# Kernel tuning notes

Measured on AMD Instinct MI355X. Metric: run time of the kernel, lower is better.

Reference implementation:

```python
import jax, jax.numpy as jnp
import numpy as np

EPS_KNN = 1e-12
EPS_COS = 1e-8


def setup_inputs() -> dict:
    key = jax.random.key(0)
    ks = jax.random.split(key, 12)
    B, N, D, H = 2048, 50000, 3, 512
    z = jax.random.normal(ks[0], (B, D + 3), jnp.float32)
    t = jax.random.uniform(ks[1], (), jnp.float32)
    x0 = jax.random.normal(ks[2], (N, D), jnp.float32)
    x1 = jax.random.normal(ks[3], (N, D), jnp.float32)
    v0 = jax.random.normal(ks[4], (N, D), jnp.float32)
    v1 = jax.random.normal(ks[5], (N, D), jnp.float32)
    # MLP model: (D+1) -> H -> H -> D
    W1 = jax.random.normal(ks[6], (D + 1, H), jnp.float32) * 0.1
    b1 = jnp.zeros((H,), jnp.float32)
    W2 = jax.random.normal(ks[7], (H, H), jnp.float32) * 0.05
    b2 = jnp.zeros((H,), jnp.float32)
    W3 = jax.random.normal(ks[8], (H, D), jnp.float32) * 0.05
    b3 = jnp.zeros((D,), jnp.float32)
    return {"z": z, "t": t, "x0": x0, "x1": x1, "v0": v0, "v1": v1,
            "W1": W1, "b1": b1, "W2": W2, "b2": b2, "W3": W3, "b3": b3,
            "k": 100}


def _mlp(xin, W1, b1, W2, b2, W3, b3):
    h = jax.nn.relu(xin @ W1 + b1)
    h = jax.nn.relu(h @ W2 + b2)
    return h @ W3 + b3


def _get_ut_knn_gaussian(xt, x0, x1, v0, v1, k):
    x = jnp.concatenate([x0, x1], axis=0)   # [2N, D]
    v = jnp.concatenate([v0, v1], axis=0)   # [2N, D]
    # euclidean cdist via the GEMM identity, clamped for numerical safety
    d2 = ((xt * xt).sum(1, keepdims=True)
          + (x * x).sum(1)[None, :]
          - 2.0 * xt @ x.T)                 # [B, 2N]
    dists = jnp.sqrt(jnp.maximum(d2, 0.0))
    neg_d, knn_idx = jax.lax.top_k(-dists, k)  # smallest-k, ascending in dist
    knn_dists = -neg_d                          # [B, k]
    h = jnp.maximum(knn_dists[:, -1:], EPS_KNN)  # bandwidth = k-th distance
    w = jnp.exp(-knn_dists ** 2 / (2.0 * h ** 2))
    w = w / (w.sum(1, keepdims=True) + EPS_KNN)
    v_knn = v[knn_idx]                           # [B, k, D] gather
    return jnp.einsum('bk,bkd->bd', w, v_knn)


def reference(z, t, x0, x1, v0, v1, W1, b1, W2, b2, W3, b3, k):
    x = z[:, :-3]                                 # [B, D]
    B = x.shape[0]
    t_col = jnp.full((B, 1), t, dtype=x.dtype)
    x_dot = _mlp(jnp.concatenate([x, t_col], axis=1), W1, b1, W2, b2, W3, b3)
    u_t = _get_ut_knn_gaussian(x, x0, x1, v0, v1, k)
    nu = jnp.maximum(jnp.linalg.norm(u_t, axis=1), EPS_COS)
    nd = jnp.maximum(jnp.linalg.norm(x_dot, axis=1), EPS_COS)
    cos_dist = 1.0 - (u_t * x_dot).sum(1) / (nu * nd)
    # self.cos_dist_all starts at 0, so after one call cos_dist_all == cos_dist
    cos_dist_all = cos_dist
    l2_sq = ((u_t - x_dot) ** 2).sum(1)
    return jnp.concatenate([x_dot, cos_dist_all[:, None], cos_dist[:, None], l2_sq[:, None]], axis=1)
```

## Files before the change

### kernel.cpp

```cpp
#include <hip/hip_runtime.h>
#include <math.h>

#define KTHREADS 256
#define QB 2
#define NBUCKET 2048
#define CANDMAX 1024
#define TINY 256
#define TSAMP 8u
#define EPS_KNN 1e-12f
#define EPS_COS 1e-8f
#define MQ 8

__device__ __forceinline__ float wredf(float v) {
#pragma unroll
    for (int off = 32; off > 0; off >>= 1) v += __shfl_xor(v, off, 64);
    return v;
}
__device__ __forceinline__ unsigned int wredu(unsigned int v) {
#pragma unroll
    for (int off = 32; off > 0; off >>= 1) v += (unsigned int)__shfl_xor((int)v, off, 64);
    return v;
}

__global__ __launch_bounds__(512) void mlp_kernel(
    const float* __restrict__ z, const float* __restrict__ tp,
    const float* __restrict__ W1, const float* __restrict__ b1,
    const float* __restrict__ W2, const float* __restrict__ b2,
    const float* __restrict__ W3, const float* __restrict__ b3,
    float* __restrict__ xdot, int B)
{
    __shared__ float h1[MQ][512];
    __shared__ float red[8][MQ * 3];
    const int tid = threadIdx.x, lane = tid & 63, wid = tid >> 6;
    const int qbase = blockIdx.x * MQ;
    const float t = tp[0];

    for (int idx = tid; idx < MQ * 512; idx += 512) {
        const int q = idx >> 9, j = idx & 511;
        const int qid = qbase + q;
        float v = 0.f;
        if (qid < B) {
            const float a = z[qid * 6 + 0], b = z[qid * 6 + 1], c = z[qid * 6 + 2];
            v = fmaf(a, W1[j], fmaf(b, W1[512 + j], fmaf(c, W1[1024 + j], fmaf(t, W1[1536 + j], b1[j]))));
            v = fmaxf(v, 0.f);
        }
        h1[q][j] = v;
    }
    __syncthreads();

    const int col = wid * 64 + lane;
    float acc[MQ];
#pragma unroll
    for (int q = 0; q < MQ; ++q) acc[q] = b2[col];

    float w[4], wn[4];
#pragma unroll
    for (int u = 0; u < 4; ++u) w[u] = W2[u * 512 + col];
    for (int r = 0; r < 512; r += 4) {
        const int rn = r + 4;
        if (rn < 512) {
#pragma unroll
            for (int u = 0; u < 4; ++u) wn[u] = W2[(rn + u) * 512 + col];
        }
        float4 hv[MQ];
#pragma unroll
        for (int q = 0; q < MQ; ++q) hv[q] = *(const float4*)&h1[q][r];
#pragma unroll
        for (int q = 0; q < MQ; ++q) {
            acc[q] = fmaf(hv[q].x, w[0], acc[q]);
            acc[q] = fmaf(hv[q].y, w[1], acc[q]);
            acc[q] = fmaf(hv[q].z, w[2], acc[q]);
            acc[q] = fmaf(hv[q].w, w[3], acc[q]);
        }
#pragma unroll
        for (int u = 0; u < 4; ++u) w[u] = wn[u];
    }

    const float wc0 = W3[col * 3 + 0], wc1 = W3[col * 3 + 1], wc2 = W3[col * 3 + 2];
#pragma unroll
    for (int q = 0; q < MQ; ++q) {
        const float h = fmaxf(acc[q], 0.f);
        float p0 = h * wc0, p1 = h * wc1, p2 = h * wc2;
        p0 = wredf(p0); p1 = wredf(p1); p2 = wredf(p2);
        if (lane == 0) { red[wid][q * 3 + 0] = p0; red[wid][q * 3 + 1] = p1; red[wid][q * 3 + 2] = p2; }
    }
    __syncthreads();
    if (tid < MQ * 3) {
        const int q = tid / 3, d = tid % 3;
        float s = 0.f;
#pragma unroll
        for (int w8 = 0; w8 < 8; ++w8) s += red[w8][q * 3 + d];
        const int qid = qbase + q;
        if (qid < B) xdot[qid * 3 + d] = s + b3[d];
    }
}

template<int NB>
__device__ void scan_find(const unsigned int* h, unsigned int T,
                          int* out_b, unsigned int* out_total,
                          unsigned int* wtot, int tid)
{
    constexpr int CH = NB / KTHREADS;
    const int lane = tid & 63, wid = tid >> 6;
    const int base = tid * CH;
    unsigned int s = 0;
#pragma unroll
    for (int u = 0; u < CH; ++u) s += h[base + u];
    unsigned int incl = s;
#pragma unroll
    for (int d = 1; d < 64; d <<= 1) {
        unsigned int n = (unsigned int)__shfl_up((int)incl, d, 64);
        if (lane >= d) incl += n;
    }
    if (tid == 0) *out_b = -1;
    if (lane == 63) wtot[wid] = incl;
    __syncthreads();
    unsigned int offs = 0;
    for (int w = 0; w < wid; ++w) offs += wtot[w];
    const unsigned int total = wtot[0] + wtot[1] + wtot[2] + wtot[3];
    const unsigned int excl = offs + (incl - s);
    if (excl < T && T <= excl + s) {
        unsigned int c = excl;
        for (int u = 0; u < CH; ++u) {
            c += h[base + u];
            if (c >= T) { *out_b = base + u; break; }
        }
    }
    if (tid == 0) *out_total = total;
    __syncthreads();
}

__global__ __launch_bounds__(KTHREADS) void knn_kernel(
    const float* __restrict__ z,
    const float* __restrict__ x0, const float* __restrict__ x1,
    const float* __restrict__ v0, const float* __restrict__ v1,
    const float* __restrict__ xdot, const int* __restrict__ kp,
    float* __restrict__ out, int B, int N0, int N1)
{
    const int N = N0 + N1;
    const unsigned int K = (unsigned int)kp[0];

    __shared__ unsigned int hist[QB][NBUCKET];
    float (*candD)[CANDMAX] = (float (*)[CANDMAX])&hist[0][0];
    int   (*candI)[CANDMAX] = (int (*)[CANDMAX])((char*)&hist[0][0] + sizeof(float) * QB * CANDMAX);
    __shared__ unsigned int fh[256];
    __shared__ float tinyD[TINY];
    __shared__ int   tinyI[TINY];
    __shared__ unsigned int tcnt;
    __shared__ unsigned int candCnt[QB];
    __shared__ float capv[QB];
    __shared__ float hselv[QB];
    __shared__ int   iselv[QB];
    __shared__ int   doneQ[QB];
    __shared__ int   anyleft;
    __shared__ unsigned int wtot[4];
    __shared__ int s_b;
    __shared__ unsigned int s_tot;
    __shared__ float qsh[QB][4];
    __shared__ float redbuf[4][QB * 4];

    const int tid = threadIdx.x, lane = tid & 63, wid = tid >> 6;
    const int qbase = blockIdx.x * QB;

    if (tid < QB) {
        const int qid = qbase + tid;
        float a = 0.f, b = 0.f, c = 0.f;
        if (qid < B) { a = z[qid * 6 + 0]; b = z[qid * 6 + 1]; c = z[qid * 6 + 2]; }
        qsh[tid][0] = a; qsh[tid][1] = b; qsh[tid][2] = c;
        qsh[tid][3] = fmaf(a, a, fmaf(b, b, c * c));
    }
    for (int i = tid; i < QB * NBUCKET; i += KTHREADS) (&hist[0][0])[i] = 0u;
    __syncthreads();

    float qx[QB], qy[QB], qz[QB], q2[QB];
#pragma unroll
    for (int q = 0; q < QB; ++q) { qx[q] = qsh[q][0]; qy[q] = qsh[q][1]; qz[q] = qsh[q][2]; q2[q] = qsh[q][3]; }

    auto doPoint = [&](float px, float py, float pz, int idx, auto&& fn) {
        const float p2 = fmaf(px, px, fmaf(py, py, pz * pz));
#pragma unroll
        for (int q = 0; q < QB; ++q) {
            const float dt = fmaf(qx[q], px, fmaf(qy[q], py, qz[q] * pz));
            const float d2 = fmaf(-2.f, dt, q2[q] + p2);
            fn(q, idx, d2);
        }
    };

    auto sweepArr = [&](const float* xa, int nG, int ibase, auto&& fn) {
        int g = tid;
        if (g < nG) {
            const float4* bp = (const float4*)(xa + 12 * (size_t)g);
            float4 A = bp[0], Bv = bp[1], C = bp[2];
            for (;;) {
                const int gn = g + KTHREADS;
                float4 An, Bn, Cn;
                const bool has = gn < nG;
                if (has) {
                    const float4* np = (const float4*)(xa + 12 * (size_t)gn);
                    An = np[0]; Bn = np[1]; Cn = np[2];
                }
                const int ib = ibase + 4 * g;
                doPoint(A.x, A.y, A.z, ib + 0, fn);
                doPoint(A.w, Bv.x, Bv.y, ib + 1, fn);
                doPoint(Bv.z, Bv.w, C.x, ib + 2, fn);
                doPoint(C.y, C.z, C.w, ib + 3, fn);
                if (!has) break;
                g = gn; A = An; Bv = Bn; C = Cn;
            }
        }
    };

    auto sweepAll = [&](auto&& fn) {
        const int G0 = N0 >> 2, G1 = N1 >> 2;
        sweepArr(x0, G0, 0, fn);
        for (int j = (G0 << 2) + tid; j < N0; j += KTHREADS)
            doPoint(x0[3 * j], x0[3 * j + 1], x0[3 * j + 2], j, fn);
        sweepArr(x1, G1, N0, fn);
        for (int j = (G1 << 2) + tid; j < N1; j += KTHREADS)
            doPoint(x1[3 * j], x1[3 * j + 1], x1[3 * j + 2], N0 + j, fn);
    };

    for (int s = tid; s < 2048; s += KTHREADS) {
        const int j = (int)(((long long)s * (long long)N) >> 11);
        float px, py, pz;
        if (j < N0) { px = x0[3 * j]; py = x0[3 * j + 1]; pz = x0[3 * j + 2]; }
        else { const int j2 = j - N0; px = x1[3 * j2]; py = x1[3 * j2 + 1]; pz = x1[3 * j2 + 2]; }
        const float p2 = fmaf(px, px, fmaf(py, py, pz * pz));
#pragma unroll
        for (int q = 0; q < QB; ++q) {
            const float dt = fmaf(qx[q], px, fmaf(qy[q], py, qz[q] * pz));
            float d2 = fmaf(-2.f, dt, q2[q] + p2);
            d2 = fmaxf(d2, 0.f);
            int bu = (int)(__float_as_uint(d2) >> 20);
            bu = bu < (NBUCKET - 1) ? bu : (NBUCKET - 1);
            atomicAdd(&hist[q][bu], 1u);
        }
    }
    __syncthreads();
    for (int q = 0; q < QB; ++q) {
        scan_find<NBUCKET>(&hist[q][0], TSAMP, &s_b, &s_tot, wtot, tid);
        if (tid == 0) {
            int b = s_b; if (b < 0) b = NBUCKET - 1;
            const unsigned int ub = (unsigned int)(b + 1);
            const float cap = (ub >= 2040u) ? 3.4e38f : __uint_as_float(ub << 20);
            capv[q] = (qbase + q < B) ? cap : -1.f;
            doneQ[q] = (qbase + q < B) ? 0 : 1;
        }
        __syncthreads();
    }

    for (int attempt = 0; attempt < 4; ++attempt) {
        if (tid == 0) anyleft = 0;
        if (tid < QB && !doneQ[tid]) candCnt[tid] = 0u;
        __syncthreads();
        float rcap[QB];
#pragma unroll
        for (int q = 0; q < QB; ++q) rcap[q] = doneQ[q] ? -1.f : capv[q];
        sweepAll([&](int q, int j, float d2) {
            if (d2 < rcap[q]) {
                const unsigned int pos = atomicAdd(&candCnt[q], 1u);
                if (pos < (unsigned int)CANDMAX) { candD[q][pos] = sqrtf(fmaxf(d2, 0.f)); candI[q][pos] = j; }
            }
        });
        __syncthreads();
        if (tid < QB && !doneQ[tid]) {
            const unsigned int c = candCnt[tid];
            if (c >= K && c <= (unsigned int)CANDMAX) doneQ[tid] = 1;
            else {
                const unsigned int cc = c < 8u ? 8u : c;
                capv[tid] *= __powf(384.f / (float)cc, 0.6666667f);
                anyleft = 1;
            }
        }
        __syncthreads();
        if (!anyleft) break;
    }

    for (int q = 0; q < QB; ++q) {
        if (qbase + q >= B) continue;
        const unsigned int cnt = candCnt[q];
        const int m = (int)(cnt < (unsigned int)CANDMAX ? cnt : (unsigned int)CANDMAX);
        fh[tid] = 0u;
        __syncthreads();
        const float sc = 256.f / sqrtf(capv[q]);
        for (int i = tid; i < m; i += KTHREADS) {
            int b = (int)(candD[q][i] * sc); b = b < 255 ? b : 255;
            atomicAdd(&fh[b], 1u);
        }
        __syncthreads();
        scan_find<256>(fh, K, &s_b, &s_tot, wtot, tid);
        const int bsel = s_b < 0 ? 255 : s_b;
        unsigned int v = (tid < bsel) ? fh[tid] : 0u;
        v = wredu(v);
        if (lane == 0) wtot[wid] = v;
        if (tid == 0) tcnt = 0u;
        __syncthreads();
        const unsigned int Cb = wtot[0] + wtot[1] + wtot[2] + wtot[3];
        for (int i = tid; i < m; i += KTHREADS) {
            int b = (int)(candD[q][i] * sc); b = b < 255 ? b : 255;
            if (b == bsel) {
                const unsigned int p = atomicAdd(&tcnt, 1u);
                if (p < (unsigned int)TINY) { tinyD[p] = candD[q][i]; tinyI[p] = candI[q][i]; }
            }
        }
        __syncthreads();
        const int c2 = (int)tcnt;
        const int need = (int)K - 1 - (int)Cb;
        if (c2 <= TINY) {
            for (int i = tid; i < c2; i += KTHREADS) {
                const float di = tinyD[i]; const int ii = tinyI[i];
                int r = 0;
                for (int j2 = 0; j2 < c2; ++j2) {
                    const float dj = tinyD[j2];
                    if (dj < di || (dj == di && tinyI[j2] < ii)) ++r;
                }
                if (r == need) { hselv[q] = di; iselv[q] = ii; }
            }
        } else {
            for (int i = tid; i < m; i += KTHREADS) {
                const float di = candD[q][i]; const int ii = candI[q][i];
                int r = 0;
                for (int j2 = 0; j2 < m; ++j2) {
                    const float dj = candD[q][j2];
                    if (dj < di || (dj == di && candI[q][j2] < ii)) ++r;
                }
                if (r == (int)K - 1) { hselv[q] = di; iselv[q] = ii; }
            }
        }
        __syncthreads();
    }

    for (int q = 0; q < QB; ++q) {
        if (qbase + q >= B) continue;
        const float hS = hselv[q];
        const int iS = iselv[q];
        const float hcl = fmaxf(hS, EPS_KNN);
        const float inv2h2 = 1.f / (2.f * hcl * hcl);
        const unsigned int cnt = candCnt[q];
        const int m = (int)(cnt < (unsigned int)CANDMAX ? cnt : (unsigned int)CANDMAX);
        float ws = 0.f, ax = 0.f, ay = 0.f, az = 0.f;
        for (int i = tid; i < m; i += KTHREADS) {
            const float s = candD[q][i];
            const int j = candI[q][i];
            if (s < hS || (s == hS && j <= iS)) {
                const float w = expf(-(s * s) * inv2h2);
                const float* vp = (j < N0) ? (v0 + 3 * (size_t)j) : (v1 + 3 * (size_t)(j - N0));
                ws += w;
                ax = fmaf(w, vp[0], ax);
                ay = fmaf(w, vp[1], ay);
                az = fmaf(w, vp[2], az);
            }
        }
        ws = wredf(ws); ax = wredf(ax); ay = wredf(ay); az = wredf(az);
        if (lane == 0) {
            redbuf[wid][q * 4 + 0] = ws; redbuf[wid][q * 4 + 1] = ax;
            redbuf[wid][q * 4 + 2] = ay; redbuf[wid][q * 4 + 3] = az;
        }
    }
    __syncthreads();

    if (tid < QB) {
        const int q = tid, qid = qbase + q;
        if (qid < B) {
            const float ws = redbuf[0][q*4+0] + redbuf[1][q*4+0] + redbuf[2][q*4+0] + redbuf[3][q*4+0];
            const float ax = redbuf[0][q*4+1] + redbuf[1][q*4+1] + redbuf[2][q*4+1] + redbuf[3][q*4+1];
            const float ay = redbuf[0][q*4+2] + redbuf[1][q*4+2] + redbuf[2][q*4+2] + redbuf[3][q*4+2];
            const float az = redbuf[0][q*4+3] + redbuf[1][q*4+3] + redbuf[2][q*4+3] + redbuf[3][q*4+3];
            const float inv = 1.f / (ws + EPS_KNN);
            const float ux = ax * inv, uy = ay * inv, uz = az * inv;
            const float d0 = xdot[qid * 3 + 0], d1 = xdot[qid * 3 + 1], d2v = xdot[qid * 3 + 2];
            const float nu = fmaxf(sqrtf(ux * ux + uy * uy + uz * uz), EPS_COS);
            const float nd = fmaxf(sqrtf(d0 * d0 + d1 * d1 + d2v * d2v), EPS_COS);
            const float cs = 1.f - (ux * d0 + uy * d1 + uz * d2v) / (nu * nd);
            const float ex = ux - d0, ey = uy - d1, ez = uz - d2v;
            const float l2 = ex * ex + ey * ey + ez * ez;
            out[qid * 6 + 0] = d0;
            out[qid * 6 + 1] = d1;
            out[qid * 6 + 2] = d2v;
            out[qid * 6 + 3] = cs;
            out[qid * 6 + 4] = cs;
            out[qid * 6 + 5] = l2;
        }
    }
}

extern "C" void kernel_launch(void* const* d_in, const int* in_sizes, int n_in,
                              void* d_out, int out_size, void* d_ws, size_t ws_size,
                              hipStream_t stream)
{
    const float* z  = (const float*)d_in[0];
    const float* tp = (const float*)d_in[1];
    const float* x0 = (const float*)d_in[2];
    const float* x1 = (const float*)d_in[3];
    const float* v0 = (const float*)d_in[4];
    const float* v1 = (const float*)d_in[5];
    const float* W1 = (const float*)d_in[6];
    const float* b1 = (const float*)d_in[7];
    const float* W2 = (const float*)d_in[8];
    const float* b2 = (const float*)d_in[9];
    const float* W3 = (const float*)d_in[10];
    const float* b3 = (const float*)d_in[11];
    const int*   kp = (const int*)d_in[12];
    float* outp = (float*)d_out;
    const int B  = in_sizes[0] / 6;
    const int N0 = in_sizes[2] / 3;
    const int N1 = in_sizes[3] / 3;
    float* xdot = (float*)d_ws;

    hipLaunchKernelGGL(mlp_kernel, dim3((B + MQ - 1) / MQ), dim3(512), 0, stream,
                       z, tp, W1, b1, W2, b2, W3, b3, xdot, B);
    hipLaunchKernelGGL(knn_kernel, dim3((B + QB - 1) / QB), dim3(KTHREADS), 0, stream,
                       z, x0, x1, v0, v1, xdot, kp, outp, B, N0, N1);
}
```

Baseline: 302.5 us.

## Pack reference points into float4 with precomputed norms and batch four queries per block

Adds a pre-pass kernel that packs x0 and x1 into one float4 array holding xyz plus the squared norm, so each KNN sweep does one aligned vector load per point and skips recomputing the norm. The KNN kernel also now handles four queries per block instead of two, so each pass over the points serves twice as many queries and fewer blocks are launched. The packed path only runs when the workspace is large enough; otherwise it falls back to the old path. Doubling the queries per block doubles the shared histogram and candidate arrays, which may reduce occupancy, and the new layout adds an extra kernel launch plus more memory traffic per point (16 bytes instead of 12).

```diff
diff --git a/kernel.cpp b/kernel.cpp
--- a/kernel.cpp
+++ b/kernel.cpp
@@ -2,7 +2,7 @@
 #include <math.h>
 
 #define KTHREADS 256
-#define QB 2
+#define QB 4
 #define NBUCKET 2048
 #define CANDMAX 1024
 #define TINY 256
@@ -20,6 +20,19 @@
 #pragma unroll
     for (int off = 32; off > 0; off >>= 1) v += (unsigned int)__shfl_xor((int)v, off, 64);
     return v;
+}
+
+__global__ __launch_bounds__(256) void pack_kernel(
+    const float* __restrict__ x0, const float* __restrict__ x1,
+    float4* __restrict__ pts, int N0, int N)
+{
+    const int i = blockIdx.x * 256 + threadIdx.x;
+    if (i >= N) return;
+    float px, py, pz;
+    if (i < N0) { px = x0[3 * i]; py = x0[3 * i + 1]; pz = x0[3 * i + 2]; }
+    else { const int j = i - N0; px = x1[3 * j]; py = x1[3 * j + 1]; pz = x1[3 * j + 2]; }
+    const float p2 = fmaf(px, px, fmaf(py, py, pz * pz));
+    pts[i] = make_float4(px, py, pz, p2);
 }
 
 __global__ __launch_bounds__(512) void mlp_kernel(
@@ -130,9 +143,11 @@
     __syncthreads();
 }
 
+template<bool PACKED>
 __global__ __launch_bounds__(KTHREADS) void knn_kernel(
     const float* __restrict__ z,
     const float* __restrict__ x0, const float* __restrict__ x1,
+    const float4* __restrict__ pts,
     const float* __restrict__ v0, const float* __restrict__ v1,
     const float* __restrict__ xdot, const int* __restrict__ kp,
     float* __restrict__ out, int B, int N0, int N1)
@@ -176,13 +191,45 @@
 #pragma unroll
     for (int q = 0; q < QB; ++q) { qx[q] = qsh[q][0]; qy[q] = qsh[q][1]; qz[q] = qsh[q][2]; q2[q] = qsh[q][3]; }
 
-    auto doPoint = [&](float px, float py, float pz, int idx, auto&& fn) {
-        const float p2 = fmaf(px, px, fmaf(py, py, pz * pz));
+    auto perPoint = [&](float px, float py, float pz, float p2, int idx, auto&& fn) {
 #pragma unroll
         for (int q = 0; q < QB; ++q) {
             const float dt = fmaf(qx[q], px, fmaf(qy[q], py, qz[q] * pz));
             const float d2 = fmaf(-2.f, dt, q2[q] + p2);
             fn(q, idx, d2);
+        }
+    };
+    auto doPointRaw = [&](float px, float py, float pz, int idx, auto&& fn) {
+        const float p2 = fmaf(px, px, fmaf(py, py, pz * pz));
+        perPoint(px, py, pz, p2, idx, fn);
+    };
+
+    auto sweepPacked = [&](auto&& fn) {
+        const int NB_main = (N >> 10) << 10;
+        if (NB_main > 0) {
+            float4 P[4], Pn[4];
+#pragma unroll
+            for (int u = 0; u < 4; ++u) P[u] = pts[tid + (u << 8)];
+            int base = 0;
+            for (;;) {
+                const int nb = base + 1024;
+                const bool has = nb < NB_main;
+                if (has) {
+#pragma unroll
+                    for (int u = 0; u < 4; ++u) Pn[u] = pts[nb + tid + (u << 8)];
+                }
+#pragma unroll
+                for (int u = 0; u < 4; ++u)
+                    perPoint(P[u].x, P[u].y, P[u].z, P[u].w, base + tid + (u << 8), fn);
+                if (!has) break;
+                base = nb;
+#pragma unroll
+                for (int u = 0; u < 4; ++u) P[u] = Pn[u];
+            }
+        }
+        for (int j = NB_main + tid; j < N; j += KTHREADS) {
+            const float4 P = pts[j];
+            perPoint(P.x, P.y, P.z, P.w, j, fn);
         }
     };
 
@@ -200,10 +247,10 @@
                     An = np[0]; Bn = np[1]; Cn = np[2];
                 }
                 const int ib = ibase + 4 * g;
-                doPoint(A.x, A.y, A.z, ib + 0, fn);
-                doPoint(A.w, Bv.x, Bv.y, ib + 1, fn);
-                doPoint(Bv.z, Bv.w, C.x, ib + 2, fn);
-                doPoint(C.y, C.z, C.w, ib + 3, fn);
+                doPointRaw(A.x, A.y, A.z, ib + 0, fn);
+                doPointRaw(A.w, Bv.x, Bv.y, ib + 1, fn);
+                doPointRaw(Bv.z, Bv.w, C.x, ib + 2, fn);
+                doPointRaw(C.y, C.z, C.w, ib + 3, fn);
                 if (!has) break;
                 g = gn; A = An; Bv = Bn; C = Cn;
             }
@@ -211,21 +258,27 @@
     };
 
     auto sweepAll = [&](auto&& fn) {
+        if (PACKED) { sweepPacked(fn); return; }
         const int G0 = N0 >> 2, G1 = N1 >> 2;
         sweepArr(x0, G0, 0, fn);
         for (int j = (G0 << 2) + tid; j < N0; j += KTHREADS)
-            doPoint(x0[3 * j], x0[3 * j + 1], x0[3 * j + 2], j, fn);
+            doPointRaw(x0[3 * j], x0[3 * j + 1], x0[3 * j + 2], j, fn);
         sweepArr(x1, G1, N0, fn);
         for (int j = (G1 << 2) + tid; j < N1; j += KTHREADS)
-            doPoint(x1[3 * j], x1[3 * j + 1], x1[3 * j + 2], N0 + j, fn);
+            doPointRaw(x1[3 * j], x1[3 * j + 1], x1[3 * j + 2], N0 + j, fn);
     };
 
     for (int s = tid; s < 2048; s += KTHREADS) {
         const int j = (int)(((long long)s * (long long)N) >> 11);
-        float px, py, pz;
-        if (j < N0) { px = x0[3 * j]; py = x0[3 * j + 1]; pz = x0[3 * j + 2]; }
-        else { const int j2 = j - N0; px = x1[3 * j2]; py = x1[3 * j2 + 1]; pz = x1[3 * j2 + 2]; }
-        const float p2 = fmaf(px, px, fmaf(py, py, pz * pz));
+        float px, py, pz, p2;
+        if (PACKED) {
+            const float4 P = pts[j];
+            px = P.x; py = P.y; pz = P.z; p2 = P.w;
+        } else {
+            if (j < N0) { px = x0[3 * j]; py = x0[3 * j + 1]; pz = x0[3 * j + 2]; }
+            else { const int j2 = j - N0; px = x1[3 * j2]; py = x1[3 * j2 + 1]; pz = x1[3 * j2 + 2]; }
+            p2 = fmaf(px, px, fmaf(py, py, pz * pz));
+        }
 #pragma unroll
         for (int q = 0; q < QB; ++q) {
             const float dt = fmaf(qx[q], px, fmaf(qy[q], py, qz[q] * pz));
@@ -405,10 +458,22 @@
     const int B  = in_sizes[0] / 6;
     const int N0 = in_sizes[2] / 3;
     const int N1 = in_sizes[3] / 3;
+    const int N  = N0 + N1;
+
     float* xdot = (float*)d_ws;
+    const size_t xdot_bytes = ((size_t)B * 3 * sizeof(float) + 15) & ~(size_t)15;
+    float4* pts = (float4*)((char*)d_ws + xdot_bytes);
+    const bool packed = ws_size >= xdot_bytes + (size_t)N * sizeof(float4);
 
     hipLaunchKernelGGL(mlp_kernel, dim3((B + MQ - 1) / MQ), dim3(512), 0, stream,
                        z, tp, W1, b1, W2, b2, W3, b3, xdot, B);
-    hipLaunchKernelGGL(knn_kernel, dim3((B + QB - 1) / QB), dim3(KTHREADS), 0, stream,
-                       z, x0, x1, v0, v1, xdot, kp, outp, B, N0, N1);
-}
+    if (packed) {
+        hipLaunchKernelGGL(pack_kernel, dim3((N + 255) / 256), dim3(256), 0, stream,
+                           x0, x1, pts, N0, N);
+        hipLaunchKernelGGL((knn_kernel<true>), dim3((B + QB - 1) / QB), dim3(KTHREADS), 0, stream,
+                           z, x0, x1, pts, v0, v1, xdot, kp, outp, B, N0, N1);
+    } else {
+        hipLaunchKernelGGL((knn_kernel<false>), dim3((B + QB - 1) / QB), dim3(KTHREADS), 0, stream,
+                           z, x0, x1, pts, v0, v1, xdot, kp, outp, B, N0, N1);
+    }
+}
```

Result: slower. 368.1 us (+21.7%).

## Split kNN into pack, sample, sliced sweep and finalize kernels via workspace

Applied to the files above, without the earlier changes.

Replaces the monolithic per-block kNN kernel with a pipeline. First the points are packed into float4 with the precomputed squared norm. Next a sampling kernel estimates a per-query distance cap. A sweep kernel then processes 8 queries per block with the point set split into 4 slices, appending candidates to global buffers with atomics. A final kernel selects the k-th distance and does the weighted gather, rescanning all points for a query when its candidate count is out of range. This aims to raise parallelism and reuse each point load across more queries, at the cost of global atomics, extra launches and a workspace-size dependency; the old kernel stays as a fallback when the workspace is too small.

```diff
diff --git a/kernel.cpp b/kernel.cpp
--- a/kernel.cpp
+++ b/kernel.cpp
@@ -1,15 +1,20 @@
 #include <hip/hip_runtime.h>
 #include <math.h>
 
-#define KTHREADS 256
-#define QB 2
+#define KT 256
+#define QA 8
+#define SLICES 4
+#define QS 8
+#define QBF 4
+#define CANDPQ 1024
 #define NBUCKET 2048
-#define CANDMAX 1024
 #define TINY 256
 #define TSAMP 8u
 #define EPS_KNN 1e-12f
 #define EPS_COS 1e-8f
 #define MQ 8
+#define QB 2
+#define CANDMAX 1024
 
 __device__ __forceinline__ float wredf(float v) {
 #pragma unroll
@@ -20,79 +25,6 @@
 #pragma unroll
     for (int off = 32; off > 0; off >>= 1) v += (unsigned int)__shfl_xor((int)v, off, 64);
     return v;
-}
-
-__global__ __launch_bounds__(512) void mlp_kernel(
-    const float* __restrict__ z, const float* __restrict__ tp,
-    const float* __restrict__ W1, const float* __restrict__ b1,
-    const float* __restrict__ W2, const float* __restrict__ b2,
-    const float* __restrict__ W3, const float* __restrict__ b3,
-    float* __restrict__ xdot, int B)
-{
-    __shared__ float h1[MQ][512];
-    __shared__ float red[8][MQ * 3];
-    const int tid = threadIdx.x, lane = tid & 63, wid = tid >> 6;
-    const int qbase = blockIdx.x * MQ;
-    const float t = tp[0];
-
-    for (int idx = tid; idx < MQ * 512; idx += 512) {
-        const int q = idx >> 9, j = idx & 511;
-        const int qid = qbase + q;
-        float v = 0.f;
-        if (qid < B) {
-            const float a = z[qid * 6 + 0], b = z[qid * 6 + 1], c = z[qid * 6 + 2];
-            v = fmaf(a, W1[j], fmaf(b, W1[512 + j], fmaf(c, W1[1024 + j], fmaf(t, W1[1536 + j], b1[j]))));
-            v = fmaxf(v, 0.f);
-        }
-        h1[q][j] = v;
-    }
-    __syncthreads();
-
-    const int col = wid * 64 + lane;
-    float acc[MQ];
-#pragma unroll
-    for (int q = 0; q < MQ; ++q) acc[q] = b2[col];
-
-    float w[4], wn[4];
-#pragma unroll
-    for (int u = 0; u < 4; ++u) w[u] = W2[u * 512 + col];
-    for (int r = 0; r < 512; r += 4) {
-        const int rn = r + 4;
-        if (rn < 512) {
-#pragma unroll
-            for (int u = 0; u < 4; ++u) wn[u] = W2[(rn + u) * 512 + col];
-        }
-        float4 hv[MQ];
-#pragma unroll
-        for (int q = 0; q < MQ; ++q) hv[q] = *(const float4*)&h1[q][r];
-#pragma unroll
-        for (int q = 0; q < MQ; ++q) {
-            acc[q] = fmaf(hv[q].x, w[0], acc[q]);
-            acc[q] = fmaf(hv[q].y, w[1], acc[q]);
-            acc[q] = fmaf(hv[q].z, w[2], acc[q]);
-            acc[q] = fmaf(hv[q].w, w[3], acc[q]);
-        }
-#pragma unroll
-        for (int u = 0; u < 4; ++u) w[u] = wn[u];
-    }
-
-    const float wc0 = W3[col * 3 + 0], wc1 = W3[col * 3 + 1], wc2 = W3[col * 3 + 2];
-#pragma unroll
-    for (int q = 0; q < MQ; ++q) {
-        const float h = fmaxf(acc[q], 0.f);
-        float p0 = h * wc0, p1 = h * wc1, p2 = h * wc2;
-        p0 = wredf(p0); p1 = wredf(p1); p2 = wredf(p2);
-        if (lane == 0) { red[wid][q * 3 + 0] = p0; red[wid][q * 3 + 1] = p1; red[wid][q * 3 + 2] = p2; }
-    }
-    __syncthreads();
-    if (tid < MQ * 3) {
-        const int q = tid / 3, d = tid % 3;
-        float s = 0.f;
-#pragma unroll
-        for (int w8 = 0; w8 < 8; ++w8) s += red[w8][q * 3 + d];
-        const int qid = qbase + q;
-        if (qid < B) xdot[qid * 3 + d] = s + b3[d];
-    }
 }
 
 template<int NB>
@@ -100,7 +32,7 @@
                           int* out_b, unsigned int* out_total,
                           unsigned int* wtot, int tid)
 {
-    constexpr int CH = NB / KTHREADS;
+    constexpr int CH = NB / KT;
     const int lane = tid & 63, wid = tid >> 6;
     const int base = tid * CH;
     unsigned int s = 0;
@@ -130,7 +62,319 @@
     __syncthreads();
 }
 
-__global__ __launch_bounds__(KTHREADS) void knn_kernel(
+__global__ __launch_bounds__(256) void pack_kernel(
+    const float* __restrict__ x0, const float* __restrict__ x1,
+    float4* __restrict__ pts, int N0, int N)
+{
+    const int i = blockIdx.x * 256 + threadIdx.x;
+    if (i >= N) return;
+    float px, py, pz;
+    if (i < N0) { px = x0[3 * i]; py = x0[3 * i + 1]; pz = x0[3 * i + 2]; }
+    else { const int j = i - N0; px = x1[3 * j]; py = x1[3 * j + 1]; pz = x1[3 * j + 2]; }
+    const float p2 = fmaf(px, px, fmaf(py, py, pz * pz));
+    pts[i] = make_float4(px, py, pz, p2);
+}
+
+__global__ __launch_bounds__(512) void mlp_kernel(
+    const float* __restrict__ z, const float* __restrict__ tp,
+    const float* __restrict__ W1, const float* __restrict__ b1,
+    const float* __restrict__ W2, const float* __restrict__ b2,
+    const float* __restrict__ W3, const float* __restrict__ b3,
+    float* __restrict__ xdot, int B)
+{
+    __shared__ float h1[MQ][512];
+    __shared__ float red[8][MQ * 3];
+    const int tid = threadIdx.x, lane = tid & 63, wid = tid >> 6;
+    const int qbase = blockIdx.x * MQ;
+    const float t = tp[0];
+
+    for (int idx = tid; idx < MQ * 512; idx += 512) {
+        const int q = idx >> 9, j = idx & 511;
+        const int qid = qbase + q;
+        float v = 0.f;
+        if (qid < B) {
+            const float a = z[qid * 6 + 0], b = z[qid * 6 + 1], c = z[qid * 6 + 2];
+            v = fmaf(a, W1[j], fmaf(b, W1[512 + j], fmaf(c, W1[1024 + j], fmaf(t, W1[1536 + j], b1[j]))));
+            v = fmaxf(v, 0.f);
+        }
+        h1[q][j] = v;
+    }
+    __syncthreads();
+
+    const int col = wid * 64 + lane;
+    float acc[MQ];
+#pragma unroll
+    for (int q = 0; q < MQ; ++q) acc[q] = b2[col];
+
+    float w[4], wn[4];
+#pragma unroll
+    for (int u = 0; u < 4; ++u) w[u] = W2[u * 512 + col];
+    for (int r = 0; r < 512; r += 4) {
+        const int rn = r + 4;
+        if (rn < 512) {
+#pragma unroll
+            for (int u = 0; u < 4; ++u) wn[u] = W2[(rn + u) * 512 + col];
+        }
+        float4 hv[MQ];
+#pragma unroll
+        for (int q = 0; q < MQ; ++q) hv[q] = *(const float4*)&h1[q][r];
+#pragma unroll
+        for (int q = 0; q < MQ; ++q) {
+            acc[q] = fmaf(hv[q].x, w[0], acc[q]);
+            acc[q] = fmaf(hv[q].y, w[1], acc[q]);
+            acc[q] = fmaf(hv[q].z, w[2], acc[q]);
+            acc[q] = fmaf(hv[q].w, w[3], acc[q]);
+        }
+#pragma unroll
+        for (int u = 0; u < 4; ++u) w[u] = wn[u];
+    }
+
+    const float wc0 = W3[col * 3 + 0], wc1 = W3[col * 3 + 1], wc2 = W3[col * 3 + 2];
+#pragma unroll
+    for (int q = 0; q < MQ; ++q) {
+        const float h = fmaxf(acc[q], 0.f);
+        float p0 = h * wc0, p1 = h * wc1, p2 = h * wc2;
+        p0 = wredf(p0); p1 = wredf(p1); p2 = wredf(p2);
+        if (lane == 0) { red[wid][q * 3 + 0] = p0; red[wid][q * 3 + 1] = p1; red[wid][q * 3 + 2] = p2; }
+    }
+    __syncthreads();
+    if (tid < MQ * 3) {
+        const int q = tid / 3, d = tid % 3;
+        float s = 0.f;
+#pragma unroll
+        for (int w8 = 0; w8 < 8; ++w8) s += red[w8][q * 3 + d];
+        const int qid = qbase + q;
+        if (qid < B) xdot[qid * 3 + d] = s + b3[d];
+    }
+}
+
+__global__ __launch_bounds__(KT) void sample_kernel(
+    const float* __restrict__ z, const float4* __restrict__ pts,
+    float* __restrict__ capg, unsigned int* __restrict__ gcnt,
+    int B, int N)
+{
+    __shared__ unsigned int hist[NBUCKET];
+    __shared__ unsigned int wtot[4];
+    __shared__ int s_b; __shared__ unsigned int s_tot;
+    const int tid = threadIdx.x;
+    const int q0 = blockIdx.x * QS;
+    if (tid < QS && q0 + tid < B) gcnt[q0 + tid] = 0u;
+    for (int u = 0; u < QS; ++u) {
+        const int qid = q0 + u;
+        for (int i = tid; i < NBUCKET; i += KT) hist[i] = 0u;
+        __syncthreads();
+        if (qid < B) {
+            const float a = z[qid * 6 + 0], b = z[qid * 6 + 1], c = z[qid * 6 + 2];
+            const float q2 = fmaf(a, a, fmaf(b, b, c * c));
+            for (int s = tid; s < 2048; s += KT) {
+                const int j = (int)(((long long)s * (long long)N) >> 11);
+                const float4 P = pts[j];
+                const float dt = fmaf(a, P.x, fmaf(b, P.y, c * P.z));
+                float d2 = fmaf(-2.f, dt, q2 + P.w);
+                d2 = fmaxf(d2, 0.f);
+                int bu = (int)(__float_as_uint(d2) >> 20);
+                bu = bu < (NBUCKET - 1) ? bu : (NBUCKET - 1);
+                atomicAdd(&hist[bu], 1u);
+            }
+        }
+        __syncthreads();
+        scan_find<NBUCKET>(hist, TSAMP, &s_b, &s_tot, wtot, tid);
+        if (tid == 0 && qid < B) {
+            int bb = s_b; if (bb < 0) bb = NBUCKET - 1;
+            const unsigned int ub = (unsigned int)(bb + 1);
+            capg[qid] = (ub >= 2040u) ? 3.4e38f : __uint_as_float(ub << 20);
+        }
+        __syncthreads();
+    }
+}
+
+__global__ __launch_bounds__(KT) void sweepA_kernel(
+    const float* __restrict__ z, const float4* __restrict__ pts,
+    const float* __restrict__ capg, unsigned int* __restrict__ gcnt,
+    float* __restrict__ gD, int* __restrict__ gI, int B, int N)
+{
+    const int tid = threadIdx.x;
+    const int slice = blockIdx.x % SLICES;
+    const int qg = blockIdx.x / SLICES;
+    const int q0 = qg * QA;
+    float qx[QA], qy[QA], qz[QA], q2[QA], cp[QA];
+#pragma unroll
+    for (int u = 0; u < QA; ++u) {
+        const int qid = q0 + u;
+        float a = 0.f, b = 0.f, c = 0.f, cap = -1.f;
+        if (qid < B) { a = z[qid * 6 + 0]; b = z[qid * 6 + 1]; c = z[qid * 6 + 2]; cap = capg[qid]; }
+        qx[u] = a; qy[u] = b; qz[u] = c; q2[u] = fmaf(a, a, fmaf(b, b, c * c)); cp[u] = cap;
+    }
+    const int slen = (N + SLICES - 1) / SLICES;
+    const int s0 = slice * slen;
+    const int s1 = min(N, s0 + slen);
+    int j = s0 + tid;
+    bool v = j < s1;
+    float4 P;
+    if (v) P = pts[j];
+    while (v) {
+        const int jn = j + KT;
+        const bool vn = jn < s1;
+        float4 Pn;
+        if (vn) Pn = pts[jn];
+#pragma unroll
+        for (int u = 0; u < QA; ++u) {
+            const float dt = fmaf(qx[u], P.x, fmaf(qy[u], P.y, qz[u] * P.z));
+            const float d2 = fmaf(-2.f, dt, q2[u] + P.w);
+            if (d2 < cp[u]) {
+                const unsigned int pos = atomicAdd(&gcnt[q0 + u], 1u);
+                if (pos < (unsigned int)CANDPQ) {
+                    gD[(size_t)(q0 + u) * CANDPQ + pos] = sqrtf(fmaxf(d2, 0.f));
+                    gI[(size_t)(q0 + u) * CANDPQ + pos] = j;
+                }
+            }
+        }
+        j = jn; v = vn; P = Pn;
+    }
+}
+
+__global__ __launch_bounds__(KT) void finalB_kernel(
+    const float* __restrict__ z, const float4* __restrict__ pts,
+    const float* __restrict__ v0, const float* __restrict__ v1,
+    const float* __restrict__ xdot, const int* __restrict__ kp,
+    const float* __restrict__ capg, const unsigned int* __restrict__ gcnt,
+    const float* __restrict__ gD, const int* __restrict__ gI,
+    float* __restrict__ out, int B, int N0, int N1)
+{
+    const int N = N0 + N1;
+    const unsigned int K = (unsigned int)kp[0];
+    __shared__ float candL[CANDPQ];
+    __shared__ int   candIL[CANDPQ];
+    __shared__ unsigned int fh[256];
+    __shared__ float tinyD[TINY];
+    __shared__ int   tinyI[TINY];
+    __shared__ unsigned int tcnt, lcnt;
+    __shared__ unsigned int wtot[4];
+    __shared__ int s_b; __shared__ unsigned int s_tot;
+    __shared__ float redbuf[4][4];
+    __shared__ float s_hsel; __shared__ int s_isel;
+    const int tid = threadIdx.x, lane = tid & 63, wid = tid >> 6;
+
+    for (int u = 0; u < QBF; ++u) {
+        const int qid = blockIdx.x * QBF + u;
+        if (qid >= B) continue;
+        const unsigned int cnt = gcnt[qid];
+        const float capq = capg[qid];
+        const float* Dp; const int* Ip; int m; float sc;
+        const bool fast = (cnt >= K && cnt <= (unsigned int)CANDPQ);
+        if (fast) {
+            Dp = gD + (size_t)qid * CANDPQ; Ip = gI + (size_t)qid * CANDPQ;
+            m = (int)cnt; sc = 256.f / sqrtf(capq);
+        } else {
+            const float a = z[qid * 6 + 0], b = z[qid * 6 + 1], c = z[qid * 6 + 2];
+            const float q2 = fmaf(a, a, fmaf(b, b, c * c));
+            float capL = capq;
+            unsigned int cc = cnt;
+            for (int att = 0; att < 6; ++att) {
+                const unsigned int base = cc < 8u ? 8u : cc;
+                capL *= __powf(384.f / (float)base, 0.6666667f);
+                if (tid == 0) lcnt = 0u;
+                __syncthreads();
+                for (int jj = tid; jj < N; jj += KT) {
+                    const float4 P = pts[jj];
+                    const float dt = fmaf(a, P.x, fmaf(b, P.y, c * P.z));
+                    const float d2 = fmaf(-2.f, dt, q2 + P.w);
+                    if (d2 < capL) {
+                        const unsigned int pos = atomicAdd(&lcnt, 1u);
+                        if (pos < (unsigned int)CANDPQ) { candL[pos] = sqrtf(fmaxf(d2, 0.f)); candIL[pos] = jj; }
+                    }
+                }
+                __syncthreads();
+                cc = lcnt;
+                if (cc >= K && cc <= (unsigned int)CANDPQ) break;
+            }
+            Dp = candL; Ip = candIL;
+            m = (int)(cc <= (unsigned int)CANDPQ ? cc : (unsigned int)CANDPQ);
+            sc = 256.f / sqrtf(capL);
+        }
+        fh[tid] = 0u;
+        __syncthreads();
+        for (int i = tid; i < m; i += KT) {
+            int bb = (int)(Dp[i] * sc); bb = bb < 255 ? bb : 255;
+            atomicAdd(&fh[bb], 1u);
+        }
+        __syncthreads();
+        scan_find<256>(fh, K, &s_b, &s_tot, wtot, tid);
+        const int bsel = s_b < 0 ? 255 : s_b;
+        unsigned int vv = (tid < bsel) ? fh[tid] : 0u;
+        vv = wredu(vv);
+        if (lane == 0) wtot[wid] = vv;
+        if (tid == 0) { tcnt = 0u; s_hsel = 3.4e38f; s_isel = 0x7fffffff; }
+        __syncthreads();
+        const unsigned int Cb = wtot[0] + wtot[1] + wtot[2] + wtot[3];
+        for (int i = tid; i < m; i += KT) {
+            int bb = (int)(Dp[i] * sc); bb = bb < 255 ? bb : 255;
+            if (bb == bsel) {
+                const unsigned int p = atomicAdd(&tcnt, 1u);
+                if (p < (unsigned int)TINY) { tinyD[p] = Dp[i]; tinyI[p] = Ip[i]; }
+            }
+        }
+        __syncthreads();
+        const int c2 = (int)tcnt;
+        const int need = (int)K - 1 - (int)Cb;
+        if (c2 <= TINY) {
+            for (int i = tid; i < c2; i += KT) {
+                const float di = tinyD[i]; const int ii = tinyI[i];
+                int r = 0;
+                for (int j2 = 0; j2 < c2; ++j2) {
+                    const float dj = tinyD[j2];
+                    if (dj < di || (dj == di && tinyI[j2] < ii)) ++r;
+                }
+                if (r == need) { s_hsel = di; s_isel = ii; }
+            }
+        } else {
+            for (int i = tid; i < m; i += KT) {
+                const float di = Dp[i]; const int ii = Ip[i];
+                int r = 0;
+                for (int j2 = 0; j2 < m; ++j2) {
+                    const float dj = Dp[j2];
+                    if (dj < di || (dj == di && Ip[j2] < ii)) ++r;
+                }
+                if (r == (int)K - 1) { s_hsel = di; s_isel = ii; }
+            }
+        }
+        __syncthreads();
+        const float hS = s_hsel; const int iS = s_isel;
+        const float hcl = fmaxf(hS, EPS_KNN);
+        const float inv2h2 = 1.f / (2.f * hcl * hcl);
+        float ws = 0.f, ax = 0.f, ay = 0.f, az = 0.f;
+        for (int i = tid; i < m; i += KT) {
+            const float s = Dp[i]; const int jj = Ip[i];
+            if (s < hS || (s == hS && jj <= iS)) {
+                const float w = expf(-(s * s) * inv2h2);
+                const float* vp = (jj < N0) ? (v0 + 3 * (size_t)jj) : (v1 + 3 * (size_t)(jj - N0));
+                ws += w; ax = fmaf(w, vp[0], ax); ay = fmaf(w, vp[1], ay); az = fmaf(w, vp[2], az);
+            }
+        }
+        ws = wredf(ws); ax = wredf(ax); ay = wredf(ay); az = wredf(az);
+        if (lane == 0) { redbuf[wid][0] = ws; redbuf[wid][1] = ax; redbuf[wid][2] = ay; redbuf[wid][3] = az; }
+        __syncthreads();
+        if (tid == 0) {
+            const float wsum = redbuf[0][0] + redbuf[1][0] + redbuf[2][0] + redbuf[3][0];
+            const float axs  = redbuf[0][1] + redbuf[1][1] + redbuf[2][1] + redbuf[3][1];
+            const float ays  = redbuf[0][2] + redbuf[1][2] + redbuf[2][2] + redbuf[3][2];
+            const float azs  = redbuf[0][3] + redbuf[1][3] + redbuf[2][3] + redbuf[3][3];
+            const float inv = 1.f / (wsum + EPS_KNN);
+            const float ux = axs * inv, uy = ays * inv, uz = azs * inv;
+            const float d0 = xdot[qid * 3 + 0], d1 = xdot[qid * 3 + 1], d2v = xdot[qid * 3 + 2];
+            const float nu = fmaxf(sqrtf(ux * ux + uy * uy + uz * uz), EPS_COS);
+            const float nd = fmaxf(sqrtf(d0 * d0 + d1 * d1 + d2v * d2v), EPS_COS);
+            const float cs = 1.f - (ux * d0 + uy * d1 + uz * d2v) / (nu * nd);
+            const float ex = ux - d0, ey = uy - d1, ez = uz - d2v;
+            const float l2 = ex * ex + ey * ey + ez * ez;
+            out[qid * 6 + 0] = d0; out[qid * 6 + 1] = d1; out[qid * 6 + 2] = d2v;
+            out[qid * 6 + 3] = cs; out[qid * 6 + 4] = cs; out[qid * 6 + 5] = l2;
+        }
+        __syncthreads();
+    }
+}
+
+__global__ __launch_bounds__(KT) void knn_fallback(
     const float* __restrict__ z,
     const float* __restrict__ x0, const float* __restrict__ x1,
     const float* __restrict__ v0, const float* __restrict__ v1,
@@ -139,7 +383,6 @@
 {
     const int N = N0 + N1;
     const unsigned int K = (unsigned int)kp[0];
-
     __shared__ unsigned int hist[QB][NBUCKET];
     float (*candD)[CANDMAX] = (float (*)[CANDMAX])&hist[0][0];
     int   (*candI)[CANDMAX] = (int (*)[CANDMAX])((char*)&hist[0][0] + sizeof(float) * QB * CANDMAX);
@@ -158,7 +401,6 @@
     __shared__ unsigned int s_tot;
     __shared__ float qsh[QB][4];
     __shared__ float redbuf[4][QB * 4];
-
     const int tid = threadIdx.x, lane = tid & 63, wid = tid >> 6;
     const int qbase = blockIdx.x * QB;
 
@@ -169,9 +411,8 @@
         qsh[tid][0] = a; qsh[tid][1] = b; qsh[tid][2] = c;
         qsh[tid][3] = fmaf(a, a, fmaf(b, b, c * c));
     }
-    for (int i = tid; i < QB * NBUCKET; i += KTHREADS) (&hist[0][0])[i] = 0u;
+    for (int i = tid; i < QB * NBUCKET; i += KT) (&hist[0][0])[i] = 0u;
     __syncthreads();
-
     float qx[QB], qy[QB], qz[QB], q2[QB];
 #pragma unroll
     for (int q = 0; q < QB; ++q) { qx[q] = qsh[q][0]; qy[q] = qsh[q][1]; qz[q] = qsh[q][2]; q2[q] = qsh[q][3]; }
@@ -185,42 +426,32 @@
             fn(q, idx, d2);
         }
     };
-
-    auto sweepArr = [&](const float* xa, int nG, int ibase, auto&& fn) {
-        int g = tid;
-        if (g < nG) {
-            const float4* bp = (const float4*)(xa + 12 * (size_t)g);
-            float4 A = bp[0], Bv = bp[1], C = bp[2];
-            for (;;) {
-                const int gn = g + KTHREADS;
-                float4 An, Bn, Cn;
-                const bool has = gn < nG;
-                if (has) {
-                    const float4* np = (const float4*)(xa + 12 * (size_t)gn);
-                    An = np[0]; Bn = np[1]; Cn = np[2];
-                }
-                const int ib = ibase + 4 * g;
-                doPoint(A.x, A.y, A.z, ib + 0, fn);
-                doPoint(A.w, Bv.x, Bv.y, ib + 1, fn);
-                doPoint(Bv.z, Bv.w, C.x, ib + 2, fn);
-                doPoint(C.y, C.z, C.w, ib + 3, fn);
-                if (!has) break;
-                g = gn; A = An; Bv = Bn; C = Cn;
-            }
-        }
-    };
-
     auto sweepAll = [&](auto&& fn) {
-        const int G0 = N0 >> 2, G1 = N1 >> 2;
-        sweepArr(x0, G0, 0, fn);
-        for (int j = (G0 << 2) + tid; j < N0; j += KTHREADS)
+        const int G0 = N0 >> 2;
+        for (int g = tid; g < G0; g += KT) {
+            const float4* bp = (const float4*)(x0 + 12 * (size_t)g);
+            const float4 A = bp[0], Bv = bp[1], C = bp[2];
+            doPoint(A.x, A.y, A.z, 4 * g + 0, fn);
+            doPoint(A.w, Bv.x, Bv.y, 4 * g + 1, fn);
+            doPoint(Bv.z, Bv.w, C.x, 4 * g + 2, fn);
+            doPoint(C.y, C.z, C.w, 4 * g + 3, fn);
+        }
+        for (int j = (G0 << 2) + tid; j < N0; j += KT)
             doPoint(x0[3 * j], x0[3 * j + 1], x0[3 * j + 2], j, fn);
-        sweepArr(x1, G1, N0, fn);
-        for (int j = (G1 << 2) + tid; j < N1; j += KTHREADS)
+        const int G1 = N1 >> 2;
+        for (int g = tid; g < G1; g += KT) {
+            const float4* bp = (const float4*)(x1 + 12 * (size_t)g);
+            const float4 A = bp[0], Bv = bp[1], C = bp[2];
+            doPoint(A.x, A.y, A.z, N0 + 4 * g + 0, fn);
+            doPoint(A.w, Bv.x, Bv.y, N0 + 4 * g + 1, fn);
+            doPoint(Bv.z, Bv.w, C.x, N0 + 4 * g + 2, fn);
+            doPoint(C.y, C.z, C.w, N0 + 4 * g + 3, fn);
+        }
+        for (int j = (G1 << 2) + tid; j < N1; j += KT)
             doPoint(x1[3 * j], x1[3 * j + 1], x1[3 * j + 2], N0 + j, fn);
     };
 
-    for (int s = tid; s < 2048; s += KTHREADS) {
+    for (int s = tid; s < 2048; s += KT) {
         const int j = (int)(((long long)s * (long long)N) >> 11);
         float px, py, pz;
         if (j < N0) { px = x0[3 * j]; py = x0[3 * j + 1]; pz = x0[3 * j + 2]; }
@@ -248,7 +479,6 @@
         }
         __syncthreads();
     }
-
     for (int attempt = 0; attempt < 4; ++attempt) {
         if (tid == 0) anyleft = 0;
         if (tid < QB && !doneQ[tid]) candCnt[tid] = 0u;
@@ -275,7 +505,6 @@
         __syncthreads();
         if (!anyleft) break;
     }
-
     for (int q = 0; q < QB; ++q) {
         if (qbase + q >= B) continue;
         const unsigned int cnt = candCnt[q];
@@ -283,7 +512,7 @@
         fh[tid] = 0u;
         __syncthreads();
         const float sc = 256.f / sqrtf(capv[q]);
-        for (int i = tid; i < m; i += KTHREADS) {
+        for (int i = tid; i < m; i += KT) {
             int b = (int)(candD[q][i] * sc); b = b < 255 ? b : 255;
             atomicAdd(&fh[b], 1u);
         }
@@ -296,7 +525,7 @@
         if (tid == 0) tcnt = 0u;
         __syncthreads();
         const unsigned int Cb = wtot[0] + wtot[1] + wtot[2] + wtot[3];
-        for (int i = tid; i < m; i += KTHREADS) {
+        for (int i = tid; i < m; i += KT) {
             int b = (int)(candD[q][i] * sc); b = b < 255 ? b : 255;
             if (b == bsel) {
                 const unsigned int p = atomicAdd(&tcnt, 1u);
@@ -307,7 +536,7 @@
         const int c2 = (int)tcnt;
         const int need = (int)K - 1 - (int)Cb;
         if (c2 <= TINY) {
-            for (int i = tid; i < c2; i += KTHREADS) {
+            for (int i = tid; i < c2; i += KT) {
                 const float di = tinyD[i]; const int ii = tinyI[i];
                 int r = 0;
                 for (int j2 = 0; j2 < c2; ++j2) {
@@ -317,7 +546,7 @@
                 if (r == need) { hselv[q] = di; iselv[q] = ii; }
             }
         } else {
-            for (int i = tid; i < m; i += KTHREADS) {
+            for (int i = tid; i < m; i += KT) {
                 const float di = candD[q][i]; const int ii = candI[q][i];
                 int r = 0;
                 for (int j2 = 0; j2 < m; ++j2) {
@@ -329,7 +558,6 @@
         }
         __syncthreads();
     }
-
     for (int q = 0; q < QB; ++q) {
         if (qbase + q >= B) continue;
         const float hS = hselv[q];
@@ -339,16 +567,13 @@
         const unsigned int cnt = candCnt[q];
         const int m = (int)(cnt < (unsigned int)CANDMAX ? cnt : (unsigned int)CANDMAX);
         float ws = 0.f, ax = 0.f, ay = 0.f, az = 0.f;
-        for (int i = tid; i < m; i += KTHREADS) {
+        for (int i = tid; i < m; i += KT) {
             const float s = candD[q][i];
             const int j = candI[q][i];
             if (s < hS || (s == hS && j <= iS)) {
                 const float w = expf(-(s * s) * inv2h2);
                 const float* vp = (j < N0) ? (v0 + 3 * (size_t)j) : (v1 + 3 * (size_t)(j - N0));
-                ws += w;
-                ax = fmaf(w, vp[0], ax);
-                ay = fmaf(w, vp[1], ay);
-                az = fmaf(w, vp[2], az);
+                ws += w; ax = fmaf(w, vp[0], ax); ay = fmaf(w, vp[1], ay); az = fmaf(w, vp[2], az);
             }
         }
         ws = wredf(ws); ax = wredf(ax); ay = wredf(ay); az = wredf(az);
@@ -358,7 +583,6 @@
         }
     }
     __syncthreads();
-
     if (tid < QB) {
         const int q = tid, qid = qbase + q;
         if (qid < B) {
@@ -374,12 +598,8 @@
             const float cs = 1.f - (ux * d0 + uy * d1 + uz * d2v) / (nu * nd);
             const float ex = ux - d0, ey = uy - d1, ez = uz - d2v;
             const float l2 = ex * ex + ey * ey + ez * ez;
-            out[qid * 6 + 0] = d0;
-            out[qid * 6 + 1] = d1;
-            out[qid * 6 + 2] = d2v;
-            out[qid * 6 + 3] = cs;
-            out[qid * 6 + 4] = cs;
-            out[qid * 6 + 5] = l2;
+            out[qid * 6 + 0] = d0; out[qid * 6 + 1] = d1; out[qid * 6 + 2] = d2v;
+            out[qid * 6 + 3] = cs; out[qid * 6 + 4] = cs; out[qid * 6 + 5] = l2;
         }
     }
 }
@@ -405,10 +625,39 @@
     const int B  = in_sizes[0] / 6;
     const int N0 = in_sizes[2] / 3;
     const int N1 = in_sizes[3] / 3;
-    float* xdot = (float*)d_ws;
+    const int N  = N0 + N1;
+
+    size_t off = 0;
+    auto alloc = [&](size_t bytes) { size_t o = off; off = (off + bytes + 255) & ~(size_t)255; return o; };
+    const size_t o_xdot = alloc((size_t)B * 3 * sizeof(float));
+    const size_t o_pts  = alloc((size_t)N * sizeof(float4));
+    const size_t o_cap  = alloc((size_t)B * sizeof(float));
+    const size_t o_cnt  = alloc((size_t)B * sizeof(unsigned int));
+    const size_t o_gD   = alloc((size_t)B * CANDPQ * sizeof(float));
+    const size_t o_gI   = alloc((size_t)B * CANDPQ * sizeof(int));
+    const bool split = ws_size >= off;
+
+    float* xdot = (float*)((char*)d_ws + o_xdot);
 
     hipLaunchKernelGGL(mlp_kernel, dim3((B + MQ - 1) / MQ), dim3(512), 0, stream,
                        z, tp, W1, b1, W2, b2, W3, b3, xdot, B);
-    hipLaunchKernelGGL(knn_kernel, dim3((B + QB - 1) / QB), dim3(KTHREADS), 0, stream,
-                       z, x0, x1, v0, v1, xdot, kp, outp, B, N0, N1);
-}
+    if (split) {
+        float4* pts = (float4*)((char*)d_ws + o_pts);
+        float* capg = (float*)((char*)d_ws + o_cap);
+        unsigned int* gcnt = (unsigned int*)((char*)d_ws + o_cnt);
+        float* gD = (float*)((char*)d_ws + o_gD);
+        int*   gI = (int*)((char*)d_ws + o_gI);
+        const int QG = (B + QA - 1) / QA;
+        hipLaunchKernelGGL(pack_kernel, dim3((N + 255) / 256), dim3(256), 0, stream,
+                           x0, x1, pts, N0, N);
+        hipLaunchKernelGGL(sample_kernel, dim3((B + QS - 1) / QS), dim3(KT), 0, stream,
+                           z, pts, capg, gcnt, B, N);
+        hipLaunchKernelGGL(sweepA_kernel, dim3(QG * SLICES), dim3(KT), 0, stream,
+                           z, pts, capg, gcnt, gD, gI, B, N);
+        hipLaunchKernelGGL(finalB_kernel, dim3((B + QBF - 1) / QBF), dim3(KT), 0, stream,
+                           z, pts, v0, v1, xdot, kp, capg, gcnt, gD, gI, outp, B, N0, N1);
+    } else {
+        hipLaunchKernelGGL(knn_fallback, dim3((B + QB - 1) / QB), dim3(KT), 0, stream,
+                           z, x0, x1, v0, v1, xdot, kp, outp, B, N0, N1);
+    }
+}
```

New measurement: 480.2 us. 58.8% more time.
